# Kernel tuning notes

Measured on AMD Instinct MI355X. Metric: run time of the kernel, lower is better.

## Reference

```python
import jax, jax.numpy as jnp
import numpy as np

DN = ('NCDHW', 'OIDHW', 'NCDHW')

def conv3d(x, w, b=None):
    y = jax.lax.conv_general_dilated(x, w, (1, 1, 1), 'SAME', dimension_numbers=DN)
    if b is not None:
        y = y + b[None, :, None, None, None]
    return y

def adaptive_conv(x, w):
    # x: [N,C,D,H,W], w: [N,27,D,H,W] (L1-normalized over channel dim)
    D, H, W = x.shape[2], x.shape[3], x.shape[4]
    p = jnp.pad(x, ((0, 0), (0, 0), (1, 1), (1, 1), (1, 1)))
    out = jnp.zeros_like(x)
    for i in range(3):
        for j in range(3):
            for k in range(3):
                t = i * 9 + j * 3 + k
                out = out + p[:, :, i:i + D, j:j + H, k:k + W] * w[:, t:t + 1]
    return out

def l1_normalize(w):
    # torch F.normalize(dim=1, p=1): denom clamped to 1e-12
    denom = jnp.maximum(jnp.sum(jnp.abs(w), axis=1, keepdims=True), 1e-12)
    return w / denom

def adaptive_block(x, w1, b1, w2, weights_src=None):
    src = x if weights_src is None else weights_src
    h = jax.nn.relu(conv3d(src, w1, b1))
    w = l1_normalize(conv3d(h, w2))  # [N,27,D,H,W]
    for _ in range(3):
        x = adaptive_conv(x, w)
    return x

def setup_inputs() -> dict:
    key = jax.random.key(0)
    ks = jax.random.split(key, 16)
    s = 0.05
    inp = {
        'x': jax.random.normal(ks[0], (1, 8, 128, 128, 128), dtype=jnp.float32),
        'ac1_w1': jax.random.normal(ks[1], (8, 8, 3, 3, 3), dtype=jnp.float32) * s,
        'ac1_b1': jnp.zeros((8,), dtype=jnp.float32),
        'ac1_w2': jax.random.normal(ks[2], (27, 8, 3, 3, 3), dtype=jnp.float32) * s,
        'ac2_w1': jax.random.normal(ks[3], (8, 8, 3, 3, 3), dtype=jnp.float32) * s,
        'ac2_b1': jnp.zeros((8,), dtype=jnp.float32),
        'ac2_w2': jax.random.normal(ks[4], (27, 8, 3, 3, 3), dtype=jnp.float32) * s,
        'ac3_w1': jax.random.normal(ks[5], (8, 8, 3, 3, 3), dtype=jnp.float32) * s,
        'ac3_b1': jnp.zeros((8,), dtype=jnp.float32),
        'ac3_w2': jax.random.normal(ks[6], (27, 8, 3, 3, 3), dtype=jnp.float32) * s,
        'mid_w': jax.random.normal(ks[7], (8, 8, 3, 3, 3), dtype=jnp.float32) * s,
        'mid_b': jnp.zeros((8,), dtype=jnp.float32),
        'out_w': jax.random.normal(ks[8], (1, 8, 3, 3, 3), dtype=jnp.float32) * s,
        'out_b': jnp.zeros((1,), dtype=jnp.float32),
    }
    return inp

def reference(x, ac1_w1, ac1_b1, ac1_w2, ac2_w1, ac2_b1, ac2_w2,
              ac3_w1, ac3_b1, ac3_w2, mid_w, mid_b, out_w, out_b):
    mid = adaptive_block(x, ac1_w1, ac1_b1, ac1_w2)
    mid = conv3d(mid, mid_w, mid_b)
    mid = adaptive_block(mid, ac2_w1, ac2_b1, ac2_w2)
    final = conv3d(mid, out_w, out_b)  # [N,1,D,H,W]
    final = adaptive_block(final, ac3_w1, ac3_b1, ac3_w2, weights_src=mid)
    return jnp.tanh(final)
```

## Files before the change

### kernel.cpp

```cpp
#include <hip/hip_runtime.h>
#include <math.h>

#define DSZ 128
#define VOX (DSZ*DSZ*DSZ)
#define PD  130

typedef _Float16 half8 __attribute__((ext_vector_type(8)));
typedef _Float16 half4 __attribute__((ext_vector_type(4)));
typedef _Float16 half2v __attribute__((ext_vector_type(2)));
typedef float float4v __attribute__((ext_vector_type(4)));


template<int CH>
__global__ __launch_bounds__(256) void zero_halo(_Float16* __restrict__ P)
{
    const int t = blockIdx.x * 256 + threadIdx.x;
    if (t >= PD * PD) return;
    const int zp = t / PD;
    const int yp = t - zp * PD;
    _Float16* row = P + (size_t)t * PD * CH;
    if (zp == 0 || zp == PD - 1 || yp == 0 || yp == PD - 1) {
        if (CH == 8) {
            half8 zz = {};
            for (int x = 0; x < PD; ++x) *(half8*)&row[x * 8] = zz;
        } else {
            for (int x = 0; x < PD; ++x) row[x] = (_Float16)0.0f;
        }
    } else {
        if (CH == 8) {
            half8 zz = {};
            *(half8*)&row[0] = zz;
            *(half8*)&row[(PD - 1) * 8] = zz;
        } else {
            row[0] = (_Float16)0.0f;
            row[PD - 1] = (_Float16)0.0f;
        }
    }
}

__global__ __launch_bounds__(256) void preformat(const float* __restrict__ w1a, const float* __restrict__ w1b,
                                                 const float* __restrict__ w1c, const float* __restrict__ outw,
                                                 const float* __restrict__ midw,
                                                 const float* __restrict__ w2a, const float* __restrict__ w2b,
                                                 const float* __restrict__ w2c, _Float16* __restrict__ WF)
{
    const int bid = blockIdx.x, tid = threadIdx.x;
    const float* src;
    _Float16* dst;
    int nelem, sz;
    if (bid < 3)       { src = bid == 0 ? w1a : bid == 1 ? w1b : w1c; dst = WF + bid * 3712; nelem = 8 * 216; sz = 16 * 29; }
    else if (bid == 3) { src = outw; dst = WF + 3 * 3712; nelem = 216;     sz = 16 * 29; }
    else if (bid == 4) { src = midw; dst = WF + 4 * 3712; nelem = 8 * 216; sz = 16 * 29; }
    else               { src = bid == 5 ? w2a : bid == 6 ? w2b : w2c; dst = WF + 5 * 3712 + (bid - 5) * 7424; nelem = 27 * 216; sz = 32 * 29; }
    for (int i = tid; i < sz; i += 256) ((half8*)dst)[i] = half8{};
    __syncthreads();
    for (int i = tid; i < nelem; i += 256) {
        const int oc = i / 216;
        const int rem = i - oc * 216;
        const int ic = rem / 27;
        const int tap = rem - ic * 27;
        dst[(oc * 29 + tap) * 8 + ic] = (_Float16)src[i];
    }
}

__global__ __launch_bounds__(256) void cast_hp(const float* __restrict__ in,
                                               _Float16* __restrict__ hp)
{
    const int idx = blockIdx.x * 256 + threadIdx.x;
    const int w = idx & 127;
    const int h = (idx >> 7) & 127;
    const int d = idx >> 14;
    half8 v;
    #pragma unroll
    for (int ic = 0; ic < 8; ++ic) v[ic] = (_Float16)in[(size_t)ic * VOX + idx];
    const int slot = ((d + 1) * PD + (h + 1)) * PD + (w + 1);
    *(half8*)&hp[(size_t)slot * 8] = v;
}

template<bool RELU>
__global__ __launch_bounds__(256) void conv8x8_mfma(const _Float16* __restrict__ DP,
                                                    const _Float16* __restrict__ WF,
                                                    const float* __restrict__ bias,
                                                    _Float16* __restrict__ HO)
{
    __shared__ _Float16 Wr[16 * 29 * 8];
    const int tid = threadIdx.x;
    for (int i = tid; i < 16 * 29; i += 256) ((half8*)Wr)[i] = ((const half8*)WF)[i];
    __syncthreads();

    const int b = ((blockIdx.x & 7) << 10) | (blockIdx.x >> 3);
    const int h0 = (b & 63) << 1;
    const int d  = b >> 6;
    const int lane = tid & 63;
    const int wv   = tid >> 6;
    const int col  = lane & 15;
    const int q    = lane >> 4;

    half8 af[7];
    #pragma unroll
    for (int c = 0; c < 7; ++c)
        af[c] = *(const half8*)&Wr[(col * 29 + (c * 4 + q)) * 8];

    const int base0 = ((d + 1) * PD + (h0 + 1)) * PD + 1 + wv * 32 + col;
    const _Float16* p[7];
    #pragma unroll
    for (int c = 0; c < 7; ++c) {
        const int tap = min(c * 4 + q, 26);
        const int dz = tap / 9, r9 = tap - dz * 9;
        const int dy = r9 / 3,  dx = r9 - dy * 3;
        p[c] = DP + (size_t)(base0 + ((dz - 1) * PD + (dy - 1)) * PD + (dx - 1)) * 8;
    }

    #pragma unroll
    for (int r = 0; r < 2; ++r) {
        #pragma unroll
        for (int t2 = 0; t2 < 2; ++t2) {
            float4v acc = {0.0f, 0.0f, 0.0f, 0.0f};
            #pragma unroll
            for (int c = 0; c < 7; ++c) {
                const half8 bv = *(const half8*)(p[c] + (r * PD + t2 * 16) * 8);
                acc = __builtin_amdgcn_mfma_f32_16x16x32_f16(af[c], bv, acc, 0, 0, 0);
            }
            if (q < 2) {
                const float4v bl = ((const float4v*)bias)[q];
                half4 hv;
                #pragma unroll
                for (int rr = 0; rr < 4; ++rr) {
                    float v = acc[rr] + bl[rr];
                    if (RELU) v = fmaxf(v, 0.0f);
                    hv[rr] = (_Float16)v;
                }
                *(half4*)&HO[(size_t)(base0 + r * PD + t2 * 16) * 8 + q * 4] = hv;
            }
        }
    }
}

__global__ __launch_bounds__(256) void conv8x1_mfma(const _Float16* __restrict__ DP,
                                                    const _Float16* __restrict__ WF,
                                                    const float* __restrict__ bias,
                                                    _Float16* __restrict__ F)
{
    __shared__ _Float16 Wr[16 * 29 * 8];
    const int tid = threadIdx.x;
    for (int i = tid; i < 16 * 29; i += 256) ((half8*)Wr)[i] = ((const half8*)WF)[i];
    __syncthreads();

    const int b = ((blockIdx.x & 7) << 10) | (blockIdx.x >> 3);
    const int h0 = (b & 63) << 1;
    const int d  = b >> 6;
    const int lane = tid & 63;
    const int wv   = tid >> 6;
    const int col  = lane & 15;
    const int q    = lane >> 4;

    half8 af[7];
    #pragma unroll
    for (int c = 0; c < 7; ++c)
        af[c] = *(const half8*)&Wr[(col * 29 + (c * 4 + q)) * 8];

    const int base0 = ((d + 1) * PD + (h0 + 1)) * PD + 1 + wv * 32 + col;
    const _Float16* p[7];
    #pragma unroll
    for (int c = 0; c < 7; ++c) {
        const int tap = min(c * 4 + q, 26);
        const int dz = tap / 9, r9 = tap - dz * 9;
        const int dy = r9 / 3,  dx = r9 - dy * 3;
        p[c] = DP + (size_t)(base0 + ((dz - 1) * PD + (dy - 1)) * PD + (dx - 1)) * 8;
    }

    const float b0 = bias[0];
    #pragma unroll
    for (int r = 0; r < 2; ++r) {
        #pragma unroll
        for (int t2 = 0; t2 < 2; ++t2) {
            float4v acc = {0.0f, 0.0f, 0.0f, 0.0f};
            #pragma unroll
            for (int c = 0; c < 7; ++c) {
                const half8 bv = *(const half8*)(p[c] + (r * PD + t2 * 16) * 8);
                acc = __builtin_amdgcn_mfma_f32_16x16x32_f16(af[c], bv, acc, 0, 0, 0);
            }
            if (q == 0)
                F[base0 + r * PD + t2 * 16] = (_Float16)(acc[0] + b0);
        }
    }
}

__global__ __launch_bounds__(256) void conv8x27n_mfma(const _Float16* __restrict__ HP,
                                                      const _Float16* __restrict__ WF,
                                                      _Float16* __restrict__ WB)
{
    __shared__ _Float16 T[3 * 6 * 130 * 8];
    const int tid = threadIdx.x;

    const int b = ((blockIdx.x & 7) << 9) | (blockIdx.x >> 3);
    const int h0 = (b & 31) << 2;
    const int d  = b >> 5;

    for (int i = tid; i < 3 * 6 * 130; i += 256) {
        const int dz  = i / 780;
        const int rem = i - dz * 780;
        const int yy  = rem / 130;
        const int xs  = rem - yy * 130;
        ((half8*)T)[i] =
            *(const half8*)&HP[((size_t)((d + dz) * PD + (h0 + yy)) * PD + xs) * 8];
    }

    const int lane = tid & 63;
    const int wv   = tid >> 6;
    const int col  = lane & 15;
    const int q    = lane >> 4;

    half8 af[2][7];
    #pragma unroll
    for (int t = 0; t < 2; ++t)
        #pragma unroll
        for (int c = 0; c < 7; ++c)
            af[t][c] = *(const half8*)&WF[((t * 16 + col) * 29 + (c * 4 + q)) * 8];

    int lb[7];
    #pragma unroll
    for (int c = 0; c < 7; ++c) {
        const int tap = min(c * 4 + q, 26);
        const int dz = tap / 9, r9 = tap - dz * 9;
        const int dy = r9 / 3,  dx = r9 - dy * 3;
        lb[c] = ((dz * 6 + dy) * 130 + wv * 32 + col + dx) * 8;
    }

    __syncthreads();

    #pragma unroll
    for (int r = 0; r < 4; ++r) {
        #pragma unroll
        for (int t2 = 0; t2 < 2; ++t2) {
            float4v acc0 = {0.0f, 0.0f, 0.0f, 0.0f};
            float4v acc1 = {0.0f, 0.0f, 0.0f, 0.0f};
            #pragma unroll
            for (int c = 0; c < 7; ++c) {
                const half8 bv = *(const half8*)&T[lb[c] + (r * 130 + t2 * 16) * 8];
                acc0 = __builtin_amdgcn_mfma_f32_16x16x32_f16(af[0][c], bv, acc0, 0, 0, 0);
                acc1 = __builtin_amdgcn_mfma_f32_16x16x32_f16(af[1][c], bv, acc1, 0, 0, 0);
            }

            float s = 0.0f;
            #pragma unroll
            for (int rr = 0; rr < 4; ++rr) {
                s += fabsf(acc0[rr]);
                if (16 + q * 4 + rr < 27) s += fabsf(acc1[rr]);
            }
            s += __shfl_xor(s, 16);
            s += __shfl_xor(s, 32);
            const float rcp = 1.0f / fmaxf(s, 1e-12f);

            const int vox = (d << 14) + ((h0 + r) << 7) + wv * 32 + t2 * 16 + col;
            half4 o0, o1;
            #pragma unroll
            for (int rr = 0; rr < 4; ++rr) {
                o0[rr] = (_Float16)(acc0[rr] * rcp);
                o1[rr] = (_Float16)(acc1[rr] * rcp);
            }
            *(half4*)&WB[((size_t)q * VOX + vox) * 4] = o0;
            if (q < 3)
                *(half4*)&WB[((size_t)(4 + q) * VOX + vox) * 4] = o1;
        }
    }
}

__global__ __launch_bounds__(512) void aconv8i(const _Float16* __restrict__ in,
                                               const _Float16* __restrict__ wb,
                                               _Float16* __restrict__ out)
{
    __shared__ _Float16 T[4][6 * 130 * 8];
    const int b = ((blockIdx.x & 7) << 6) | (blockIdx.x >> 3);
    const int h0 = (b & 31) << 2;
    const int d0 = (b >> 5) << 3;
    const int tid = threadIdx.x;

    auto stage = [&](int z) {
        const int slot = (z + 1) & 3;
        for (int i = tid; i < 6 * 130; i += 512) {
            const int yy = i / 130;
            const int xs = i - yy * 130;
            *(half8*)&T[slot][i * 8] =
                *(const half8*)&in[((size_t)((z + 1) * PD + (h0 + yy)) * PD + xs) * 8];
        }
    };

    stage(d0 - 1); stage(d0); stage(d0 + 1);
    __syncthreads();

    const int x  = tid & 127;
    const int ly = tid >> 7;

    for (int z = d0; z < d0 + 8; ++z) {
        if (z <= d0 + 6) stage(z + 2);

        const int idx = (z << 14) + ((h0 + ly) << 7) + x;
        half4 W[7];
        #pragma unroll
        for (int k = 0; k < 7; ++k)
            W[k] = *(const half4*)(wb + ((size_t)k * VOX + idx) * 4);

        half2v a4[4];
        #pragma unroll
        for (int j = 0; j < 4; ++j) a4[j] = half2v{};

        #pragma unroll
        for (int dz = 0; dz < 3; dz++) {
            const int slot = (z + dz) & 3;
            #pragma unroll
            for (int dy = 0; dy < 3; dy++) {
                const _Float16* rp = &T[slot][((ly + dy) * 130 + (x + 1)) * 8];
                #pragma unroll
                for (int kw = 0; kw < 3; kw++) {
                    const int tap = dz * 9 + dy * 3 + kw;
                    const _Float16 wt = W[tap >> 2][tap & 3];
                    half2v w2; w2[0] = wt; w2[1] = wt;
                    const half8 hv = *(const half8*)(rp + (kw - 1) * 8);
                    const half2v* h2 = (const half2v*)&hv;
                    #pragma unroll
                    for (int j = 0; j < 4; ++j)
                        a4[j] += h2[j] * w2;
                }
            }
        }

        const int s0 = ((z + 1) * PD + (h0 + ly + 1)) * PD + (x + 1);
        half8 o;
        #pragma unroll
        for (int j = 0; j < 4; ++j) { o[2 * j] = a4[j][0]; o[2 * j + 1] = a4[j][1]; }
        *(half8*)&out[(size_t)s0 * 8] = o;

        __syncthreads();
    }
}

template<bool TANH>
__global__ __launch_bounds__(256) void aconv1h(const _Float16* __restrict__ in,
                                               const _Float16* __restrict__ wb,
                                               _Float16* __restrict__ outh,
                                               float* __restrict__ outf)
{
    const int b = ((blockIdx.x & 7) << 10) | (blockIdx.x >> 3);
    const int idx = b * 256 + threadIdx.x;
    const int w = idx & 127;
    const int h = (idx >> 7) & 127;
    const int d = idx >> 14;

    half4 W[7];
    #pragma unroll
    for (int k = 0; k < 7; ++k)
        W[k] = *(const half4*)(wb + ((size_t)k * VOX + idx) * 4);

    const int s0 = ((d + 1) * PD + (h + 1)) * PD + (w + 1);

    float acc = 0.0f;
    #pragma unroll
    for (int dz = 0; dz < 3; dz++) {
        #pragma unroll
        for (int dy = 0; dy < 3; dy++) {
            const _Float16* rp = in + s0 + ((dz - 1) * PD + (dy - 1)) * PD;
            #pragma unroll
            for (int kw = 0; kw < 3; kw++) {
                const int tap = dz * 9 + dy * 3 + kw;
                const _Float16 wt = W[tap >> 2][tap & 3];
                acc = fmaf((float)rp[kw - 1], (float)wt, acc);
            }
        }
    }

    if (TANH) outf[idx] = tanhf(acc);
    else      outh[s0] = (_Float16)acc;
}

extern "C" void kernel_launch(void* const* d_in, const int* in_sizes, int n_in,
                              void* d_out, int out_size, void* d_ws, size_t ws_size,
                              hipStream_t stream)
{
    const float* x      = (const float*)d_in[0];
    const float* ac1_w1 = (const float*)d_in[1];
    const float* ac1_b1 = (const float*)d_in[2];
    const float* ac1_w2 = (const float*)d_in[3];
    const float* ac2_w1 = (const float*)d_in[4];
    const float* ac2_b1 = (const float*)d_in[5];
    const float* ac2_w2 = (const float*)d_in[6];
    const float* ac3_w1 = (const float*)d_in[7];
    const float* ac3_b1 = (const float*)d_in[8];
    const float* ac3_w2 = (const float*)d_in[9];
    const float* mid_w  = (const float*)d_in[10];
    const float* mid_b  = (const float*)d_in[11];
    const float* out_w  = (const float*)d_in[12];
    const float* out_b  = (const float*)d_in[13];
    float* out = (float*)d_out;

    char* ws = (char*)d_ws;
    const size_t PS8 = (size_t)PD * PD * PD * 8 * 2;
    const size_t PS1 = (size_t)PD * PD * PD * 2;
    const size_t WBsz = (size_t)VOX * 28 * 2;
    _Float16* P0 = (_Float16*)(ws);
    _Float16* P1 = (_Float16*)(ws + PS8);
    _Float16* WB = (_Float16*)(ws + 2 * PS8);
    _Float16* F1 = (_Float16*)(ws + 2 * PS8 + WBsz);
    _Float16* G1 = (_Float16*)(ws + 2 * PS8 + WBsz + PS1);
    _Float16* F2 = (_Float16*)(ws + 2 * PS8 + WBsz + 2 * PS1);
    _Float16* WF = (_Float16*)(ws + 2 * PS8 + WBsz + 3 * PS1);
    _Float16* WF8_1  = WF;
    _Float16* WF8_2  = WF + 3712;
    _Float16* WF8_3  = WF + 7424;
    _Float16* WFo    = WF + 11136;
    _Float16* WFmid  = WF + 14848;
    _Float16* WF27_1 = WF + 18560;
    _Float16* WF27_2 = WF + 25984;
    _Float16* WF27_3 = WF + 33408;

    const dim3 blk(256);
    const dim3 blkA(512);
    const dim3 gridT(VOX / 256);
    const dim3 gridM(VOX / 256);
    const dim3 gridM4(VOX / 512);
    const dim3 gridA(512);
    const dim3 gridZ((PD * PD + 255) / 256);

    zero_halo<8><<<gridZ, blk, 0, stream>>>(P0);
    zero_halo<8><<<gridZ, blk, 0, stream>>>(P1);
    zero_halo<1><<<gridZ, blk, 0, stream>>>(F1);
    zero_halo<1><<<gridZ, blk, 0, stream>>>(G1);
    zero_halo<1><<<gridZ, blk, 0, stream>>>(F2);
    preformat<<<dim3(8), blk, 0, stream>>>(ac1_w1, ac2_w1, ac3_w1, out_w, mid_w,
                                           ac1_w2, ac2_w2, ac3_w2, WF);

    cast_hp<<<gridT, blk, 0, stream>>>(x, P0);
    conv8x8_mfma<true ><<<gridM, blk, 0, stream>>>(P0, WF8_1, ac1_b1, P1);
    conv8x27n_mfma<<<gridM4, blk, 0, stream>>>(P1, WF27_1, WB);
    aconv8i<<<gridA, blkA, 0, stream>>>(P0, WB, P1);
    aconv8i<<<gridA, blkA, 0, stream>>>(P1, WB, P0);
    aconv8i<<<gridA, blkA, 0, stream>>>(P0, WB, P1);
    conv8x8_mfma<false><<<gridM, blk, 0, stream>>>(P1, WFmid, mid_b, P0);
    conv8x8_mfma<true ><<<gridM, blk, 0, stream>>>(P0, WF8_2, ac2_b1, P1);
    conv8x27n_mfma<<<gridM4, blk, 0, stream>>>(P1, WF27_2, WB);
    aconv8i<<<gridA, blkA, 0, stream>>>(P0, WB, P1);
    aconv8i<<<gridA, blkA, 0, stream>>>(P1, WB, P0);
    aconv8i<<<gridA, blkA, 0, stream>>>(P0, WB, P1);
    conv8x8_mfma<true ><<<gridM, blk, 0, stream>>>(P1, WF8_3, ac3_b1, P0);
    conv8x27n_mfma<<<gridM4, blk, 0, stream>>>(P0, WF27_3, WB);
    conv8x1_mfma<<<gridM, blk, 0, stream>>>(P1, WFo, out_b, F1);
    aconv1h<false><<<gridT, blk, 0, stream>>>(F1, WB, G1, nullptr);
    aconv1h<false><<<gridT, blk, 0, stream>>>(G1, WB, F2, nullptr);
    aconv1h<true ><<<gridT, blk, 0, stream>>>(F2, WB, nullptr, out);
}
```

Before: 708.6 us.

## Stage input halo tile in LDS for 8-channel convs, four rows per block

The conv8x8 and conv8x1 MFMA kernels now cooperatively load a 3x6x130 padded input slab into shared memory and read the 27 tap operands from it, instead of issuing per-tap global loads. Each block now computes four H rows instead of two, so the grid halves and the halo is reused across more outputs. Weights are read straight from global instead of being staged in LDS. This cuts redundant global/L2 traffic for the convolution taps, at the cost of about 37KB of LDS per block, which limits occupancy, plus an extra barrier.

```diff
diff --git a/kernel.cpp b/kernel.cpp
--- a/kernel.cpp
+++ b/kernel.cpp
@@ -83,14 +83,22 @@
                                                     const float* __restrict__ bias,
                                                     _Float16* __restrict__ HO)
 {
-    __shared__ _Float16 Wr[16 * 29 * 8];
+    __shared__ _Float16 T[3 * 6 * 130 * 8];
     const int tid = threadIdx.x;
-    for (int i = tid; i < 16 * 29; i += 256) ((half8*)Wr)[i] = ((const half8*)WF)[i];
-    __syncthreads();
-
-    const int b = ((blockIdx.x & 7) << 10) | (blockIdx.x >> 3);
-    const int h0 = (b & 63) << 1;
-    const int d  = b >> 6;
+
+    const int b = ((blockIdx.x & 7) << 9) | (blockIdx.x >> 3);
+    const int h0 = (b & 31) << 2;
+    const int d  = b >> 5;
+
+    for (int i = tid; i < 3 * 6 * 130; i += 256) {
+        const int dz  = i / 780;
+        const int rem = i - dz * 780;
+        const int yy  = rem / 130;
+        const int xs  = rem - yy * 130;
+        ((half8*)T)[i] =
+            *(const half8*)&DP[((size_t)((d + dz) * PD + (h0 + yy)) * PD + xs) * 8];
+    }
+
     const int lane = tid & 63;
     const int wv   = tid >> 6;
     const int col  = lane & 15;
@@ -99,26 +107,29 @@
     half8 af[7];
     #pragma unroll
     for (int c = 0; c < 7; ++c)
-        af[c] = *(const half8*)&Wr[(col * 29 + (c * 4 + q)) * 8];
-
-    const int base0 = ((d + 1) * PD + (h0 + 1)) * PD + 1 + wv * 32 + col;
-    const _Float16* p[7];
+        af[c] = *(const half8*)&WF[(col * 29 + (c * 4 + q)) * 8];
+
+    int lb[7];
     #pragma unroll
     for (int c = 0; c < 7; ++c) {
         const int tap = min(c * 4 + q, 26);
         const int dz = tap / 9, r9 = tap - dz * 9;
         const int dy = r9 / 3,  dx = r9 - dy * 3;
-        p[c] = DP + (size_t)(base0 + ((dz - 1) * PD + (dy - 1)) * PD + (dx - 1)) * 8;
-    }
-
-    #pragma unroll
-    for (int r = 0; r < 2; ++r) {
+        lb[c] = ((dz * 6 + dy) * 130 + wv * 32 + col + dx) * 8;
+    }
+
+    __syncthreads();
+
+    const int base0 = ((d + 1) * PD + (h0 + 1)) * PD + 1 + wv * 32 + col;
+
+    #pragma unroll
+    for (int r = 0; r < 4; ++r) {
         #pragma unroll
         for (int t2 = 0; t2 < 2; ++t2) {
             float4v acc = {0.0f, 0.0f, 0.0f, 0.0f};
             #pragma unroll
             for (int c = 0; c < 7; ++c) {
-                const half8 bv = *(const half8*)(p[c] + (r * PD + t2 * 16) * 8);
+                const half8 bv = *(const half8*)&T[lb[c] + (r * 130 + t2 * 16) * 8];
                 acc = __builtin_amdgcn_mfma_f32_16x16x32_f16(af[c], bv, acc, 0, 0, 0);
             }
             if (q < 2) {
@@ -141,14 +152,22 @@
                                                     const float* __restrict__ bias,
                                                     _Float16* __restrict__ F)
 {
-    __shared__ _Float16 Wr[16 * 29 * 8];
+    __shared__ _Float16 T[3 * 6 * 130 * 8];
     const int tid = threadIdx.x;
-    for (int i = tid; i < 16 * 29; i += 256) ((half8*)Wr)[i] = ((const half8*)WF)[i];
-    __syncthreads();
-
-    const int b = ((blockIdx.x & 7) << 10) | (blockIdx.x >> 3);
-    const int h0 = (b & 63) << 1;
-    const int d  = b >> 6;
+
+    const int b = ((blockIdx.x & 7) << 9) | (blockIdx.x >> 3);
+    const int h0 = (b & 31) << 2;
+    const int d  = b >> 5;
+
+    for (int i = tid; i < 3 * 6 * 130; i += 256) {
+        const int dz  = i / 780;
+        const int rem = i - dz * 780;
+        const int yy  = rem / 130;
+        const int xs  = rem - yy * 130;
+        ((half8*)T)[i] =
+            *(const half8*)&DP[((size_t)((d + dz) * PD + (h0 + yy)) * PD + xs) * 8];
+    }
+
     const int lane = tid & 63;
     const int wv   = tid >> 6;
     const int col  = lane & 15;
@@ -157,27 +176,30 @@
     half8 af[7];
     #pragma unroll
     for (int c = 0; c < 7; ++c)
-        af[c] = *(const half8*)&Wr[(col * 29 + (c * 4 + q)) * 8];
-
-    const int base0 = ((d + 1) * PD + (h0 + 1)) * PD + 1 + wv * 32 + col;
-    const _Float16* p[7];
+        af[c] = *(const half8*)&WF[(col * 29 + (c * 4 + q)) * 8];
+
+    int lb[7];
     #pragma unroll
     for (int c = 0; c < 7; ++c) {
         const int tap = min(c * 4 + q, 26);
         const int dz = tap / 9, r9 = tap - dz * 9;
         const int dy = r9 / 3,  dx = r9 - dy * 3;
-        p[c] = DP + (size_t)(base0 + ((dz - 1) * PD + (dy - 1)) * PD + (dx - 1)) * 8;
-    }
-
+        lb[c] = ((dz * 6 + dy) * 130 + wv * 32 + col + dx) * 8;
+    }
+
+    __syncthreads();
+
+    const int base0 = ((d + 1) * PD + (h0 + 1)) * PD + 1 + wv * 32 + col;
     const float b0 = bias[0];
-    #pragma unroll
-    for (int r = 0; r < 2; ++r) {
+
+    #pragma unroll
+    for (int r = 0; r < 4; ++r) {
         #pragma unroll
         for (int t2 = 0; t2 < 2; ++t2) {
             float4v acc = {0.0f, 0.0f, 0.0f, 0.0f};
             #pragma unroll
             for (int c = 0; c < 7; ++c) {
-                const half8 bv = *(const half8*)(p[c] + (r * PD + t2 * 16) * 8);
+                const half8 bv = *(const half8*)&T[lb[c] + (r * 130 + t2 * 16) * 8];
                 acc = __builtin_amdgcn_mfma_f32_16x16x32_f16(af[c], bv, acc, 0, 0, 0);
             }
             if (q == 0)
@@ -416,7 +438,6 @@
     const dim3 blk(256);
     const dim3 blkA(512);
     const dim3 gridT(VOX / 256);
-    const dim3 gridM(VOX / 256);
     const dim3 gridM4(VOX / 512);
     const dim3 gridA(512);
     const dim3 gridZ((PD * PD + 255) / 256);
@@ -430,20 +451,20 @@
                                            ac1_w2, ac2_w2, ac3_w2, WF);
 
     cast_hp<<<gridT, blk, 0, stream>>>(x, P0);
-    conv8x8_mfma<true ><<<gridM, blk, 0, stream>>>(P0, WF8_1, ac1_b1, P1);
+    conv8x8_mfma<true ><<<gridM4, blk, 0, stream>>>(P0, WF8_1, ac1_b1, P1);
     conv8x27n_mfma<<<gridM4, blk, 0, stream>>>(P1, WF27_1, WB);
     aconv8i<<<gridA, blkA, 0, stream>>>(P0, WB, P1);
     aconv8i<<<gridA, blkA, 0, stream>>>(P1, WB, P0);
     aconv8i<<<gridA, blkA, 0, stream>>>(P0, WB, P1);
-    conv8x8_mfma<false><<<gridM, blk, 0, stream>>>(P1, WFmid, mid_b, P0);
-    conv8x8_mfma<true ><<<gridM, blk, 0, stream>>>(P0, WF8_2, ac2_b1, P1);
+    conv8x8_mfma<false><<<gridM4, blk, 0, stream>>>(P1, WFmid, mid_b, P0);
+    conv8x8_mfma<true ><<<gridM4, blk, 0, stream>>>(P0, WF8_2, ac2_b1, P1);
     conv8x27n_mfma<<<gridM4, blk, 0, stream>>>(P1, WF27_2, WB);
     aconv8i<<<gridA, blkA, 0, stream>>>(P0, WB, P1);
     aconv8i<<<gridA, blkA, 0, stream>>>(P1, WB, P0);
     aconv8i<<<gridA, blkA, 0, stream>>>(P0, WB, P1);
-    conv8x8_mfma<true ><<<gridM, blk, 0, stream>>>(P1, WF8_3, ac3_b1, P0);
+    conv8x8_mfma<true ><<<gridM4, blk, 0, stream>>>(P1, WF8_3, ac3_b1, P0);
     conv8x27n_mfma<<<gridM4, blk, 0, stream>>>(P0, WF27_3, WB);
-    conv8x1_mfma<<<gridM, blk, 0, stream>>>(P1, WFo, out_b, F1);
+    conv8x1_mfma<<<gridM4, blk, 0, stream>>>(P1, WFo, out_b, F1);
     aconv1h<false><<<gridT, blk, 0, stream>>>(F1, WB, G1, nullptr);
     aconv1h<false><<<gridT, blk, 0, stream>>>(G1, WB, F2, nullptr);
     aconv1h<true ><<<gridT, blk, 0, stream>>>(F2, WB, nullptr, out);
```

Result: faster. 676.1 us (median of 2 runs) (-4.6%).
